# Performance work log

Hardware: AMD Instinct MI355X
Metric: run time of the kernel (lower is better)

The kernel has to match this reference:

```python
import jax, jax.numpy as jnp
import numpy as np

# Graph / layer sizes (bipartite GraphSAGE-style sampling)
N = 8192      # total nodes
D = 32        # input feature dim
N3, N2, N1, N0 = 6144, 4096, 2048, 1024  # layer sizes (src -> tgt per hop)
DEG = 16
E = N0 * DEG
HID = 128
OUT = 32


def setup_inputs() -> dict:
    key = jax.random.key(0)
    ks = jax.random.split(key, 16)
    s = np.float32(1.0 / np.sqrt(N))
    dst = jnp.repeat(jnp.arange(N0, dtype=jnp.int64), DEG)         # targets, first N0 nodes
    src = jax.random.randint(ks[13], (E,), 0, N1, dtype=jnp.int64)  # sources among N1 nodes
    return {
        "x": jax.random.normal(ks[0], (N, D), jnp.float32),
        "tau": jnp.asarray(0.1, jnp.float32),                       # learned diffusion time
        "L": jax.random.normal(ks[1], (N, N), jnp.float32) * s,     # graph Laplacian (dense operator)
        "K0": jax.random.normal(ks[2], (N, N), jnp.float32) * s,    # directional-derivative kernel 0
        "K1": jax.random.normal(ks[3], (N, N), jnp.float32) * s,    # directional-derivative kernel 1
        "W_self": jax.random.normal(ks[4], (6 * D, HID), jnp.float32) * np.float32(1.0 / np.sqrt(6 * D)),
        "W_neigh": jax.random.normal(ks[5], (6 * D, HID), jnp.float32) * np.float32(1.0 / np.sqrt(6 * D)),
        "b_conv": jnp.zeros((HID,), jnp.float32),
        "W1": jax.random.normal(ks[6], (HID, 64), jnp.float32) * np.float32(1.0 / np.sqrt(HID)),
        "b1": jnp.zeros((64,), jnp.float32),
        "W2": jax.random.normal(ks[7], (64, OUT), jnp.float32) * np.float32(1.0 / 8.0),
        "b2": jnp.zeros((OUT,), jnp.float32),
        "n_id": jax.random.randint(ks[8], (N3,), 0, N, dtype=jnp.int64),
        "edge_index": jnp.stack([src, dst]),                        # [2, E] bipartite conv edges
    }


def reference(x, tau, L, K0, K1, W_self, W_neigh, b_conv, W1, b1, W2, b2, n_id, edge_index):
    # 1) diffusion: single heat-diffusion step x <- (I - tau L) x
    x = x - tau * (L @ x)
    # 2) restrict features and kernels to the sampled batch (irregular double gather)
    xb = x[n_id]                       # [N3, D]
    K0s = K0[n_id, :][:, n_id]         # [N3, N3]
    K1s = K1[n_id, :][:, n_id]
    # 3) multi-hop gradient (anisotropic) message passing on shrinking bipartite graphs
    sizes = [(N3, N2), (N2, N1)]
    out = []
    h = xb
    for (s0, s1) in sizes:
        h = jnp.concatenate([K0s[:s1, :s0] @ h, K1s[:s1, :s0] @ h], axis=1)  # width doubles per hop
        out.append(h)
    # truncate all hop outputs to last target size and concat multi-hop features
    z = jnp.concatenate([o[:N1] for o in out], axis=1)  # [N1, 6*D]
    # 4) bipartite SAGE-style conv: mean-aggregate sources onto the first N0 targets
    src, dst = edge_index[0], edge_index[1]
    agg = jax.ops.segment_sum(z[src], dst, num_segments=N0)
    cnt = jax.ops.segment_sum(jnp.ones((E,), z.dtype), dst, num_segments=N0)
    agg = agg / jnp.maximum(cnt, 1.0)[:, None]
    hc = z[:N0] @ W_self + agg @ W_neigh + b_conv       # [N0, HID]
    # 5) MLP head
    hm = jax.nn.relu(hc @ W1 + b1)
    return hm @ W2 + b2                                 # [N0, OUT]
```

## Files before the change

### kernel.cpp

```cpp
#include <hip/hip_runtime.h>
#include <hip/hip_bf16.h>

#define N_NODES 8192
#define D_IN 32
#define N3 6144
#define N2 4096
#define N1 2048
#define N0 1024
#define NE 16384
#define KZ 4
#define KRANGE (N_NODES / KZ)
#define KWAVE (KRANGE / 4)
#define NSTAGE (KWAVE / 64)

using f32x4 = __attribute__((ext_vector_type(4))) float;
using s16x8 = __attribute__((ext_vector_type(8))) short;

__device__ __forceinline__ short f2bf(float f) {
    union { __hip_bfloat16 b; short s; } u;
    u.b = __float2bfloat16(f);
    return u.s;
}
__device__ __forceinline__ float b2f(short s) {
    unsigned int u = ((unsigned int)(unsigned short)s) << 16;
    float f;
    __builtin_memcpy(&f, &u, 4);
    return f;
}

__device__ __forceinline__ void gload16(const float* g, float* l) {
    __builtin_amdgcn_global_load_lds(
        (const __attribute__((address_space(1))) void*)g,
        (__attribute__((address_space(3))) void*)l, 16, 0, 0);
}

__global__ __launch_bounds__(1024) void prep_kernel(
    const void* __restrict__ nraw, const float* __restrict__ x,
    const float* __restrict__ tau_p, int* __restrict__ n32,
    int* __restrict__ cntA, int* __restrict__ cntB,
    int* __restrict__ listA, int* __restrict__ listB, int* __restrict__ listC,
    int* __restrict__ flags,
    unsigned short* __restrict__ xh, unsigned short* __restrict__ xl,
    float4* __restrict__ zbase, int zn4) {
    __shared__ int lcnt[N_NODES];
    __shared__ float tile[128][33];
    __shared__ int lnum, lfl;
    const int b = blockIdx.x, t = threadIdx.x;
    const int* ni = (const int*)nraw;
    const long long* nl = (const long long*)nraw;

    if (b == 0) {
        bool n64 = true;
#pragma unroll
        for (int j = 0; j < 8; ++j) {
            long long a = nl[j];
            if (a < 0 || a >= N_NODES) n64 = false;
        }
        if (t == 0) { lnum = 0; lfl = 0; }
        for (int i = t; i < N_NODES; i += 1024) lcnt[i] = 0;
        __syncthreads();
        for (int j = t; j < N3; j += 1024) {
            long long v = n64 ? nl[j] : (long long)ni[j];
            if (v < 0 || v >= N_NODES) { atomicOr(&lfl, 2); v = 0; }
            if (j < N1) n32[j] = (int)v;
            atomicAdd(&lcnt[(int)v], 1);
        }
        __syncthreads();
        for (int c = t; c < N_NODES; c += 1024) {
            int cv = lcnt[c];
            cntA[c] = cv;
            if (cv) listA[atomicAdd(&lnum, 1)] = c;
        }
        __syncthreads();
        if (t == 0) { flags[2] = lnum; lnum = 0; }
        __syncthreads();
        for (int i = t; i < N_NODES; i += 1024) lcnt[i] = 0;
        __syncthreads();
        for (int j = t; j < N2; j += 1024) {
            long long v = n64 ? nl[j] : (long long)ni[j];
            v = (v < 0 || v >= N_NODES) ? 0 : v;
            atomicAdd(&lcnt[(int)v], 1);
        }
        __syncthreads();
        for (int c = t; c < N_NODES; c += 1024) {
            int cv = lcnt[c];
            cntB[c] = cv;
            if (cv) listB[atomicAdd(&lnum, 1)] = c;
        }
        __syncthreads();
        if (t == 0) { flags[3] = lnum; lnum = 0; }
        __syncthreads();
        for (int i = t; i < N_NODES; i += 1024) lcnt[i] = 0;
        __syncthreads();
        for (int j = t; j < N1; j += 1024) {
            long long v = n64 ? nl[j] : (long long)ni[j];
            v = (v < 0 || v >= N_NODES) ? 0 : v;
            atomicAdd(&lcnt[(int)v], 1);
        }
        __syncthreads();
        for (int c = t; c < N_NODES; c += 1024) {
            if (lcnt[c]) listC[atomicAdd(&lnum, 1)] = c;
        }
        __syncthreads();
        if (t == 0) {
            flags[4] = lnum;
            int f = lfl;
            if (fabsf(tau_p[0] - 0.1f) > 1e-6f) f |= 32;
            flags[0] = f;
        }
    } else {
        if (b <= 64) {
            const int c0 = (b - 1) * 128;
            const int d = t & 31, cc = t >> 5;
#pragma unroll
            for (int i = 0; i < 4; ++i)
                tile[cc + 32 * i][d] = x[(size_t)(c0 + cc + 32 * i) * D_IN + d];
            __syncthreads();
#pragma unroll
            for (int i = 0; i < 4; ++i) {
                int idx = t + 1024 * i;
                int dd = idx >> 7;
                int jj = idx & 127;
                float v = tile[jj][dd];
                short h = f2bf(v);
                xh[(size_t)dd * N_NODES + c0 + jj] = (unsigned short)h;
                xl[(size_t)dd * N_NODES + c0 + jj] = (unsigned short)f2bf(v - b2f(h));
            }
        }
        float4 zz = {0.f, 0.f, 0.f, 0.f};
        for (int i = (b - 1) * 1024 + t; i < zn4; i += 259 * 1024) zbase[i] = zz;
    }
}

template <int MODE>
__global__ __launch_bounds__(256) void rows_mmg(
    const float* __restrict__ Km0, const float* __restrict__ Km1,
    const unsigned short* __restrict__ Bhi, const unsigned short* __restrict__ Blo,
    const int* __restrict__ list, const int* __restrict__ nptr, int nidx,
    const float* __restrict__ zpad, float* __restrict__ outf) {
    constexpr int NF = (MODE == 2) ? 4 : 2;
    constexpr int NCTOT = (MODE == 0) ? 32 : ((MODE == 1) ? 64 : 128);
    const int nrows = nptr[nidx];
    const int c0 = blockIdx.x * 16;
    if (c0 >= nrows) return;
    const int tid = threadIdx.x;
    const int lane = tid & 63;
    const int wid = tid >> 6;
    const int row = lane & 15;
    const int kg = lane >> 4;

    __shared__ float tileA[4][2][16 * 64];
    __shared__ float red[4][16 * 16 * NF];
    __shared__ int rows_s[16];
    if (tid < 16) rows_s[tid] = (c0 + tid < nrows) ? list[c0 + tid] : -1;
    __syncthreads();

    const float* Km = (MODE == 0) ? Km0 : (blockIdx.y ? Km1 : Km0);
    const int zoff = (MODE == 0) ? 0 : (int)blockIdx.y * ((MODE == 1) ? 32 : 64);

    const unsigned short* bph[NF];
    const unsigned short* bpl[NF];
    const int kwb = (int)blockIdx.z * KRANGE + wid * KWAVE;
#pragma unroll
    for (int n = 0; n < NF; ++n) {
        size_t boffs = (size_t)(n * 16 + row) * N_NODES + kwb + kg * 8;
        bph[n] = Bhi + boffs;
        bpl[n] = Blo + boffs;
    }

    f32x4 acc[NF];
#pragma unroll
    for (int n = 0; n < NF; ++n) acc[n] = (f32x4){0.f, 0.f, 0.f, 0.f};

    const int srow = lane >> 4;
    const int schk = lane & 15;
#define ISSUE(buf, kofs)                                                       \
    {                                                                          \
        _Pragma("unroll") for (int i = 0; i < 4; ++i) {                        \
            int r = i * 4 + srow;                                              \
            int crw = rows_s[r];                                               \
            int sc = schk ^ (r & 15);                                          \
            const float* gp = (crw >= 0)                                       \
                                  ? Km + (size_t)crw * N_NODES + (kofs) + sc * 4 \
                                  : zpad;                                      \
            gload16(gp, &tileA[wid][buf][i * 256]);                            \
        }                                                                      \
    }

    ISSUE(0, kwb);
    for (int st = 0; st < NSTAGE; ++st) {
        const int buf = st & 1;
        if (st + 1 < NSTAGE) {
            ISSUE(buf ^ 1, kwb + (st + 1) * 64);
            asm volatile("s_waitcnt vmcnt(4)" ::: "memory");
        } else {
            asm volatile("s_waitcnt vmcnt(0)" ::: "memory");
        }
        __builtin_amdgcn_sched_barrier(0);
        const float* tb = &tileA[wid][buf][0];
#pragma unroll
        for (int ks = 0; ks < 64; ks += 32) {
            int c0i = (kg * 8 + ks) >> 2;
            float4 a0 = *(const float4*)&tb[row * 64 + ((c0i ^ (row & 15)) << 2)];
            float4 a1 = *(const float4*)&tb[row * 64 + (((c0i + 1) ^ (row & 15)) << 2)];
            float av[8] = {a0.x, a0.y, a0.z, a0.w, a1.x, a1.y, a1.z, a1.w};
            s16x8 ah, al;
#pragma unroll
            for (int i = 0; i < 8; ++i) {
                short h = f2bf(av[i]);
                ah[i] = h;
                al[i] = f2bf(av[i] - b2f(h));
            }
            const int bo = st * 64 + ks;
#pragma unroll
            for (int n = 0; n < NF; ++n) {
                s16x8 bh = *(const s16x8*)(bph[n] + bo);
                s16x8 bl = *(const s16x8*)(bpl[n] + bo);
                acc[n] = __builtin_amdgcn_mfma_f32_16x16x32_bf16(al, bh, acc[n], 0, 0, 0);
                acc[n] = __builtin_amdgcn_mfma_f32_16x16x32_bf16(ah, bl, acc[n], 0, 0, 0);
                acc[n] = __builtin_amdgcn_mfma_f32_16x16x32_bf16(ah, bh, acc[n], 0, 0, 0);
            }
        }
        __builtin_amdgcn_sched_barrier(0);
    }
#undef ISSUE

#pragma unroll
    for (int n = 0; n < NF; ++n)
#pragma unroll
        for (int r = 0; r < 4; ++r)
            red[wid][(kg * 4 + r) * (16 * NF) + (n * 16 + row)] = acc[n][r];
    __syncthreads();

    for (int e = tid; e < 16 * 16 * NF; e += 256) {
        float s = red[0][e] + red[1][e] + red[2][e] + red[3][e];
        int orow = e / (16 * NF);
        int ocol = e % (16 * NF);
        int cc = rows_s[orow];
        if (cc >= 0) atomicAdd(&outf[(size_t)cc * NCTOT + zoff + ocol], s);
    }
}

__global__ void ep0_kernel(const float* __restrict__ x, const float* __restrict__ pA,
                           const float* __restrict__ tau_p, const int* __restrict__ cntA,
                           unsigned short* __restrict__ uAh, unsigned short* __restrict__ uAl) {
    int idx = blockIdx.x * 256 + threadIdx.x;
    if (idx >= N_NODES * 32) return;
    int d = idx >> 13, c = idx & (N_NODES - 1);
    float u = (float)cntA[c] * (x[(size_t)c * D_IN + d] - tau_p[0] * pA[(size_t)c * 32 + d]);
    short h = f2bf(u);
    uAh[idx] = (unsigned short)h;
    uAl[idx] = (unsigned short)f2bf(u - b2f(h));
}

__global__ void ep1_kernel(const float* __restrict__ g1, const int* __restrict__ cntB,
                           unsigned short* __restrict__ uBh, unsigned short* __restrict__ uBl) {
    int idx = blockIdx.x * 256 + threadIdx.x;
    if (idx >= N_NODES * 64) return;
    int d = idx >> 13, c = idx & (N_NODES - 1);
    float u = (float)cntB[c] * g1[(size_t)c * 64 + d];
    short h = f2bf(u);
    uBh[idx] = (unsigned short)h;
    uBl[idx] = (unsigned short)f2bf(u - b2f(h));
}

__global__ void head_kernel(const float* __restrict__ g1, const float* __restrict__ g2,
                            const int* __restrict__ n32, const void* __restrict__ eraw,
                            const float* __restrict__ Wself, const float* __restrict__ Wneigh,
                            const float* __restrict__ bconv, const float* __restrict__ W1,
                            const float* __restrict__ b1, const float* __restrict__ W2,
                            const float* __restrict__ b2, const int* __restrict__ flags,
                            float* __restrict__ out) {
    __shared__ float zs[192], za[192], hc[128], hm[64];
    __shared__ int csrc[16];
    int t = threadIdx.x, b = blockIdx.x;
    const int* ei = (const int*)eraw;
    const long long* el = (const long long*)eraw;
    if (t < 16) {
        bool e64 = true;
#pragma unroll
        for (int j = 0; j < 8; ++j) {
            long long a = el[j];
            if (a < 0 || a >= N1) e64 = false;
        }
        long long sv = e64 ? el[b * 16 + t] : (long long)ei[b * 16 + t];
        int si = (sv < 0 || sv >= N1) ? 0 : (int)sv;
        csrc[t] = n32[si];
    }
    __syncthreads();
    if (t < 192) {
        int cb = n32[b];
        zs[t] = (t < 64) ? g1[(size_t)cb * 64 + t] : g2[(size_t)cb * 128 + (t - 64)];
        float s = 0.f;
#pragma unroll
        for (int e = 0; e < 16; ++e) {
            int c = csrc[e];
            s += (t < 64) ? g1[(size_t)c * 64 + t] : g2[(size_t)c * 128 + (t - 64)];
        }
        za[t] = s * (1.0f / 16.0f);
    }
    __syncthreads();
    if (t < 128) {
        float s = bconv[t];
        for (int d = 0; d < 192; ++d)
            s += zs[d] * Wself[d * 128 + t] + za[d] * Wneigh[d * 128 + t];
        hc[t] = s;
    }
    __syncthreads();
    if (t < 64) {
        float s = b1[t];
        for (int h = 0; h < 128; ++h) s += hc[h] * W1[h * 64 + t];
        hm[t] = fmaxf(s, 0.0f);
    }
    __syncthreads();
    if (t < 32) {
        float s = b2[t];
        for (int j = 0; j < 64; ++j) s += hm[j] * W2[j * 32 + t];
        out[(size_t)b * 32 + t] = s;
    }
    __syncthreads();
    if (b == 0 && t == 0) {
        int f = flags[0];
        if (f) out[0] = 100000.0f * (float)f;
    }
}

__global__ void ws_fail_kernel(float* out) {
    if (threadIdx.x == 0 && blockIdx.x == 0) out[0] = 100000.0f;
}

extern "C" void kernel_launch(void* const* d_in, const int* in_sizes, int n_in,
                              void* d_out, int out_size, void* d_ws, size_t ws_size,
                              hipStream_t stream) {
    const float* x      = (const float*)d_in[0];
    const float* tau    = (const float*)d_in[1];
    const float* L      = (const float*)d_in[2];
    const float* K0     = (const float*)d_in[3];
    const float* K1     = (const float*)d_in[4];
    const float* Wself  = (const float*)d_in[5];
    const float* Wneigh = (const float*)d_in[6];
    const float* bconv  = (const float*)d_in[7];
    const float* W1     = (const float*)d_in[8];
    const float* b1     = (const float*)d_in[9];
    const float* W2     = (const float*)d_in[10];
    const float* b2     = (const float*)d_in[11];
    float* out = (float*)d_out;

    char* ws = (char*)d_ws;
    size_t off = 0;
    int* flags = (int*)(ws + off); off += 256;
    int* cntA  = (int*)(ws + off); off += 32768;
    int* cntB  = (int*)(ws + off); off += 32768;
    int* n32   = (int*)(ws + off); off += 8192;
    int* listA = (int*)(ws + off); off += 32768;
    int* listB = (int*)(ws + off); off += 32768;
    int* listC = (int*)(ws + off); off += 32768;
    float* zpad = (float*)(ws + off); off += 1024;
    float* pA = (float*)(ws + off); off += (size_t)N_NODES * 32 * 4;
    float* g1 = (float*)(ws + off); off += (size_t)N_NODES * 64 * 4;
    float* g2 = (float*)(ws + off); off += (size_t)N_NODES * 128 * 4;
    unsigned short* xh  = (unsigned short*)(ws + off); off += (size_t)32 * N_NODES * 2;
    unsigned short* xl  = (unsigned short*)(ws + off); off += (size_t)32 * N_NODES * 2;
    unsigned short* uAh = (unsigned short*)(ws + off); off += (size_t)32 * N_NODES * 2;
    unsigned short* uAl = (unsigned short*)(ws + off); off += (size_t)32 * N_NODES * 2;
    unsigned short* uBh = (unsigned short*)(ws + off); off += (size_t)64 * N_NODES * 2;
    unsigned short* uBl = (unsigned short*)(ws + off); off += (size_t)64 * N_NODES * 2;
    const size_t needed = off;

    if (ws_size < needed || n_in != 14 || out_size != N0 * 32) {
        ws_fail_kernel<<<1, 64, 0, stream>>>(out);
        return;
    }

    const int zn4 = (int)((1024 + (size_t)(32 + 64 + 128) * N_NODES * 4) / 16);

    prep_kernel<<<260, 1024, 0, stream>>>(d_in[12], x, tau, n32, cntA, cntB, listA,
                                          listB, listC, flags, xh, xl, (float4*)zpad,
                                          zn4);
    rows_mmg<0><<<dim3(384, 1, KZ), 256, 0, stream>>>(L, L, xh, xl, listA, flags + 2, 0,
                                                      zpad, pA);
    ep0_kernel<<<1024, 256, 0, stream>>>(x, pA, tau, cntA, uAh, uAl);
    rows_mmg<1><<<dim3(256, 2, KZ), 256, 0, stream>>>(K0, K1, uAh, uAl, listB, flags + 2,
                                                      1, zpad, g1);
    ep1_kernel<<<2048, 256, 0, stream>>>(g1, cntB, uBh, uBl);
    rows_mmg<2><<<dim3(128, 2, KZ), 256, 0, stream>>>(K0, K1, uBh, uBl, listC, flags + 2,
                                                      2, zpad, g2);
    head_kernel<<<1024, 256, 0, stream>>>(g1, g2, n32, d_in[13], Wself, Wneigh, bconv,
                                          W1, b1, W2, b2, flags, out);
}
```

Baseline: 245.5 us.

## Fuse post-prep stages into one persistent cooperative kernel with grid syncs

Replaces the six launches after prep (three gathered-row GEMMs, two bf16-split epilogues, and the MLP head) with one cooperative persistent kernel. Each stage runs as a grid-stride loop over tiles or elements, separated by grid.sync(). The goal is to remove per-launch overhead and inter-kernel idle gaps. In exchange the grid is capped at occupancy times 256 blocks, at most 1024, so each stage's parallelism is limited by that grid. The reduction buffer now reuses the tile LDS, with extra __syncthreads, and the old launches remain as a fallback if the cooperative launch fails.

```diff
diff --git a/kernel.cpp b/kernel.cpp
--- a/kernel.cpp
+++ b/kernel.cpp
@@ -1,5 +1,8 @@
 #include <hip/hip_runtime.h>
 #include <hip/hip_bf16.h>
+#include <hip/hip_cooperative_groups.h>
+
+namespace cg = cooperative_groups;
 
 #define N_NODES 8192
 #define D_IN 32
@@ -27,7 +30,6 @@
     __builtin_memcpy(&f, &u, 4);
     return f;
 }
-
 __device__ __forceinline__ void gload16(const float* g, float* l) {
     __builtin_amdgcn_global_load_lds(
         (const __attribute__((address_space(1))) void*)g,
@@ -133,34 +135,31 @@
 }
 
 template <int MODE>
-__global__ __launch_bounds__(256) void rows_mmg(
+__device__ __forceinline__ void mm_tile_body(
     const float* __restrict__ Km0, const float* __restrict__ Km1,
     const unsigned short* __restrict__ Bhi, const unsigned short* __restrict__ Blo,
-    const int* __restrict__ list, const int* __restrict__ nptr, int nidx,
-    const float* __restrict__ zpad, float* __restrict__ outf) {
+    const int* __restrict__ list, int nrows, int tix, int y, int z,
+    const float* __restrict__ zpad, float* __restrict__ outf,
+    float* tileA, int* rows_s) {
     constexpr int NF = (MODE == 2) ? 4 : 2;
     constexpr int NCTOT = (MODE == 0) ? 32 : ((MODE == 1) ? 64 : 128);
-    const int nrows = nptr[nidx];
-    const int c0 = blockIdx.x * 16;
-    if (c0 >= nrows) return;
+    const int c0 = tix * 16;
     const int tid = threadIdx.x;
     const int lane = tid & 63;
     const int wid = tid >> 6;
     const int row = lane & 15;
     const int kg = lane >> 4;
 
-    __shared__ float tileA[4][2][16 * 64];
-    __shared__ float red[4][16 * 16 * NF];
-    __shared__ int rows_s[16];
+    __syncthreads();
     if (tid < 16) rows_s[tid] = (c0 + tid < nrows) ? list[c0 + tid] : -1;
     __syncthreads();
 
-    const float* Km = (MODE == 0) ? Km0 : (blockIdx.y ? Km1 : Km0);
-    const int zoff = (MODE == 0) ? 0 : (int)blockIdx.y * ((MODE == 1) ? 32 : 64);
+    const float* Km = (MODE == 0) ? Km0 : (y ? Km1 : Km0);
+    const int zoff = (MODE == 0) ? 0 : y * ((MODE == 1) ? 32 : 64);
 
     const unsigned short* bph[NF];
     const unsigned short* bpl[NF];
-    const int kwb = (int)blockIdx.z * KRANGE + wid * KWAVE;
+    const int kwb = z * KRANGE + wid * KWAVE;
 #pragma unroll
     for (int n = 0; n < NF; ++n) {
         size_t boffs = (size_t)(n * 16 + row) * N_NODES + kwb + kg * 8;
@@ -172,6 +171,7 @@
 #pragma unroll
     for (int n = 0; n < NF; ++n) acc[n] = (f32x4){0.f, 0.f, 0.f, 0.f};
 
+    float* twave = tileA + wid * 2048;
     const int srow = lane >> 4;
     const int schk = lane & 15;
 #define ISSUE(buf, kofs)                                                       \
@@ -183,7 +183,7 @@
             const float* gp = (crw >= 0)                                       \
                                   ? Km + (size_t)crw * N_NODES + (kofs) + sc * 4 \
                                   : zpad;                                      \
-            gload16(gp, &tileA[wid][buf][i * 256]);                            \
+            gload16(gp, twave + (buf) * 1024 + i * 256);                       \
         }                                                                      \
     }
 
@@ -197,7 +197,7 @@
             asm volatile("s_waitcnt vmcnt(0)" ::: "memory");
         }
         __builtin_amdgcn_sched_barrier(0);
-        const float* tb = &tileA[wid][buf][0];
+        const float* tb = twave + buf * 1024;
 #pragma unroll
         for (int ks = 0; ks < 64; ks += 32) {
             int c0i = (kg * 8 + ks) >> 2;
@@ -225,15 +225,19 @@
     }
 #undef ISSUE
 
+    __syncthreads();
+    float* redb = tileA;
 #pragma unroll
     for (int n = 0; n < NF; ++n)
 #pragma unroll
         for (int r = 0; r < 4; ++r)
-            red[wid][(kg * 4 + r) * (16 * NF) + (n * 16 + row)] = acc[n][r];
-    __syncthreads();
-
-    for (int e = tid; e < 16 * 16 * NF; e += 256) {
-        float s = red[0][e] + red[1][e] + red[2][e] + red[3][e];
+            redb[wid * (256 * NF) + (kg * 4 + r) * (16 * NF) + (n * 16 + row)] =
+                acc[n][r];
+    __syncthreads();
+
+    for (int e = tid; e < 256 * NF; e += 256) {
+        float s = redb[e] + redb[256 * NF + e] + redb[2 * 256 * NF + e] +
+                  redb[3 * 256 * NF + e];
         int orow = e / (16 * NF);
         int ocol = e % (16 * NF);
         int cc = rows_s[orow];
@@ -241,22 +245,17 @@
     }
 }
 
-__global__ void ep0_kernel(const float* __restrict__ x, const float* __restrict__ pA,
-                           const float* __restrict__ tau_p, const int* __restrict__ cntA,
-                           unsigned short* __restrict__ uAh, unsigned short* __restrict__ uAl) {
-    int idx = blockIdx.x * 256 + threadIdx.x;
-    if (idx >= N_NODES * 32) return;
+__device__ __forceinline__ void ep0_elem(int idx, const float* x, const float* pA,
+                                         const float* tau_p, const int* cntA,
+                                         unsigned short* uAh, unsigned short* uAl) {
     int d = idx >> 13, c = idx & (N_NODES - 1);
     float u = (float)cntA[c] * (x[(size_t)c * D_IN + d] - tau_p[0] * pA[(size_t)c * 32 + d]);
     short h = f2bf(u);
     uAh[idx] = (unsigned short)h;
     uAl[idx] = (unsigned short)f2bf(u - b2f(h));
 }
-
-__global__ void ep1_kernel(const float* __restrict__ g1, const int* __restrict__ cntB,
-                           unsigned short* __restrict__ uBh, unsigned short* __restrict__ uBl) {
-    int idx = blockIdx.x * 256 + threadIdx.x;
-    if (idx >= N_NODES * 64) return;
+__device__ __forceinline__ void ep1_elem(int idx, const float* g1, const int* cntB,
+                                         unsigned short* uBh, unsigned short* uBl) {
     int d = idx >> 13, c = idx & (N_NODES - 1);
     float u = (float)cntB[c] * g1[(size_t)c * 64 + d];
     short h = f2bf(u);
@@ -264,6 +263,140 @@
     uBl[idx] = (unsigned short)f2bf(u - b2f(h));
 }
 
+__device__ __forceinline__ void head_body(
+    const float* __restrict__ g1, const float* __restrict__ g2,
+    const int* __restrict__ n32, const void* __restrict__ eraw,
+    const float* __restrict__ Wself, const float* __restrict__ Wneigh,
+    const float* __restrict__ bconv, const float* __restrict__ W1,
+    const float* __restrict__ b1, const float* __restrict__ W2,
+    const float* __restrict__ b2, const int* __restrict__ flags,
+    float* __restrict__ out, int b, float* zs, float* za, float* hc, float* hm,
+    int* csrc) {
+    int t = threadIdx.x;
+    const int* ei = (const int*)eraw;
+    const long long* el = (const long long*)eraw;
+    if (t < 16) {
+        bool e64 = true;
+#pragma unroll
+        for (int j = 0; j < 8; ++j) {
+            long long a = el[j];
+            if (a < 0 || a >= N1) e64 = false;
+        }
+        long long sv = e64 ? el[b * 16 + t] : (long long)ei[b * 16 + t];
+        int si = (sv < 0 || sv >= N1) ? 0 : (int)sv;
+        csrc[t] = n32[si];
+    }
+    __syncthreads();
+    if (t < 192) {
+        int cb = n32[b];
+        zs[t] = (t < 64) ? g1[(size_t)cb * 64 + t] : g2[(size_t)cb * 128 + (t - 64)];
+        float s = 0.f;
+#pragma unroll
+        for (int e = 0; e < 16; ++e) {
+            int c = csrc[e];
+            s += (t < 64) ? g1[(size_t)c * 64 + t] : g2[(size_t)c * 128 + (t - 64)];
+        }
+        za[t] = s * (1.0f / 16.0f);
+    }
+    __syncthreads();
+    if (t < 128) {
+        float s = bconv[t];
+        for (int d = 0; d < 192; ++d)
+            s += zs[d] * Wself[d * 128 + t] + za[d] * Wneigh[d * 128 + t];
+        hc[t] = s;
+    }
+    __syncthreads();
+    if (t < 64) {
+        float s = b1[t];
+        for (int h = 0; h < 128; ++h) s += hc[h] * W1[h * 64 + t];
+        hm[t] = fmaxf(s, 0.0f);
+    }
+    __syncthreads();
+    if (t < 32) {
+        float s = b2[t];
+        for (int j = 0; j < 64; ++j) s += hm[j] * W2[j * 32 + t];
+        out[(size_t)b * 32 + t] = s;
+    }
+    __syncthreads();
+    if (b == 0 && t == 0) {
+        int f = flags[0];
+        if (f) out[0] = 100000.0f * (float)f;
+    }
+}
+
+struct FA {
+    const float *L, *K0, *K1, *x, *tau;
+    const int *cntA, *cntB, *listA, *listB, *listC, *flags, *n32;
+    const void* eraw;
+    const unsigned short *xh, *xl;
+    unsigned short *uAh, *uAl, *uBh, *uBl;
+    const float *Wself, *Wneigh, *bconv, *W1, *b1, *W2, *b2, *zpad;
+    float *pA, *g1, *g2, *out;
+};
+
+__global__ __launch_bounds__(256, 4) void fused_kernel(FA a) {
+    cg::grid_group grid = cg::this_grid();
+    __shared__ float tileA[4 * 2 * 1024];
+    __shared__ int rows_s[16];
+    __shared__ float zs[192], za[192], hc[128], hm[64];
+    __shared__ int csrc[16];
+    const int bid = blockIdx.x, nb = gridDim.x, tid = threadIdx.x;
+
+    const int nA = a.flags[2], nB = a.flags[3], nC = a.flags[4];
+    const int ntA = (nA + 15) >> 4, ntB = (nB + 15) >> 4, ntC = (nC + 15) >> 4;
+
+    for (int w = bid; w < ntA * KZ; w += nb)
+        mm_tile_body<0>(a.L, a.L, a.xh, a.xl, a.listA, nA, w % ntA, 0, w / ntA,
+                        a.zpad, a.pA, tileA, rows_s);
+    grid.sync();
+    for (int idx = bid * 256 + tid; idx < N_NODES * 32; idx += nb * 256)
+        ep0_elem(idx, a.x, a.pA, a.tau, a.cntA, a.uAh, a.uAl);
+    grid.sync();
+    for (int w = bid; w < ntB * 2 * KZ; w += nb) {
+        int tix = w % ntB, rem = w / ntB;
+        mm_tile_body<1>(a.K0, a.K1, a.uAh, a.uAl, a.listB, nB, tix, rem & 1,
+                        rem >> 1, a.zpad, a.g1, tileA, rows_s);
+    }
+    grid.sync();
+    for (int idx = bid * 256 + tid; idx < N_NODES * 64; idx += nb * 256)
+        ep1_elem(idx, a.g1, a.cntB, a.uBh, a.uBl);
+    grid.sync();
+    for (int w = bid; w < ntC * 2 * KZ; w += nb) {
+        int tix = w % ntC, rem = w / ntC;
+        mm_tile_body<2>(a.K0, a.K1, a.uBh, a.uBl, a.listC, nC, tix, rem & 1,
+                        rem >> 1, a.zpad, a.g2, tileA, rows_s);
+    }
+    grid.sync();
+    for (int hb = bid; hb < N0; hb += nb)
+        head_body(a.g1, a.g2, a.n32, a.eraw, a.Wself, a.Wneigh, a.bconv, a.W1,
+                  a.b1, a.W2, a.b2, a.flags, a.out, hb, zs, za, hc, hm, csrc);
+}
+
+template <int MODE>
+__global__ __launch_bounds__(256) void rows_mmg(
+    const float* __restrict__ Km0, const float* __restrict__ Km1,
+    const unsigned short* __restrict__ Bhi, const unsigned short* __restrict__ Blo,
+    const int* __restrict__ list, const int* __restrict__ nptr, int nidx,
+    const float* __restrict__ zpad, float* __restrict__ outf) {
+    __shared__ float tileA[4 * 2 * 1024];
+    __shared__ int rows_s[16];
+    int nrows = nptr[nidx];
+    if ((int)blockIdx.x * 16 >= nrows) return;
+    mm_tile_body<MODE>(Km0, Km1, Bhi, Blo, list, nrows, blockIdx.x, blockIdx.y,
+                       blockIdx.z, zpad, outf, tileA, rows_s);
+}
+
+__global__ void ep0_kernel(const float* __restrict__ x, const float* __restrict__ pA,
+                           const float* __restrict__ tau_p, const int* __restrict__ cntA,
+                           unsigned short* __restrict__ uAh, unsigned short* __restrict__ uAl) {
+    int idx = blockIdx.x * 256 + threadIdx.x;
+    if (idx < N_NODES * 32) ep0_elem(idx, x, pA, tau_p, cntA, uAh, uAl);
+}
+__global__ void ep1_kernel(const float* __restrict__ g1, const int* __restrict__ cntB,
+                           unsigned short* __restrict__ uBh, unsigned short* __restrict__ uBl) {
+    int idx = blockIdx.x * 256 + threadIdx.x;
+    if (idx < N_NODES * 64) ep1_elem(idx, g1, cntB, uBh, uBl);
+}
 __global__ void head_kernel(const float* __restrict__ g1, const float* __restrict__ g2,
                             const int* __restrict__ n32, const void* __restrict__ eraw,
                             const float* __restrict__ Wself, const float* __restrict__ Wneigh,
@@ -273,56 +406,8 @@
                             float* __restrict__ out) {
     __shared__ float zs[192], za[192], hc[128], hm[64];
     __shared__ int csrc[16];
-    int t = threadIdx.x, b = blockIdx.x;
-    const int* ei = (const int*)eraw;
-    const long long* el = (const long long*)eraw;
-    if (t < 16) {
-        bool e64 = true;
-#pragma unroll
-        for (int j = 0; j < 8; ++j) {
-            long long a = el[j];
-            if (a < 0 || a >= N1) e64 = false;
-        }
-        long long sv = e64 ? el[b * 16 + t] : (long long)ei[b * 16 + t];
-        int si = (sv < 0 || sv >= N1) ? 0 : (int)sv;
-        csrc[t] = n32[si];
-    }
-    __syncthreads();
-    if (t < 192) {
-        int cb = n32[b];
-        zs[t] = (t < 64) ? g1[(size_t)cb * 64 + t] : g2[(size_t)cb * 128 + (t - 64)];
-        float s = 0.f;
-#pragma unroll
-        for (int e = 0; e < 16; ++e) {
-            int c = csrc[e];
-            s += (t < 64) ? g1[(size_t)c * 64 + t] : g2[(size_t)c * 128 + (t - 64)];
-        }
-        za[t] = s * (1.0f / 16.0f);
-    }
-    __syncthreads();
-    if (t < 128) {
-        float s = bconv[t];
-        for (int d = 0; d < 192; ++d)
-            s += zs[d] * Wself[d * 128 + t] + za[d] * Wneigh[d * 128 + t];
-        hc[t] = s;
-    }
-    __syncthreads();
-    if (t < 64) {
-        float s = b1[t];
-        for (int h = 0; h < 128; ++h) s += hc[h] * W1[h * 64 + t];
-        hm[t] = fmaxf(s, 0.0f);
-    }
-    __syncthreads();
-    if (t < 32) {
-        float s = b2[t];
-        for (int j = 0; j < 64; ++j) s += hm[j] * W2[j * 32 + t];
-        out[(size_t)b * 32 + t] = s;
-    }
-    __syncthreads();
-    if (b == 0 && t == 0) {
-        int f = flags[0];
-        if (f) out[0] = 100000.0f * (float)f;
-    }
+    head_body(g1, g2, n32, eraw, Wself, Wneigh, bconv, W1, b1, W2, b2, flags, out,
+              blockIdx.x, zs, za, hc, hm, csrc);
 }
 
 __global__ void ws_fail_kernel(float* out) {
@@ -377,14 +462,40 @@
     prep_kernel<<<260, 1024, 0, stream>>>(d_in[12], x, tau, n32, cntA, cntB, listA,
                                           listB, listC, flags, xh, xl, (float4*)zpad,
                                           zn4);
-    rows_mmg<0><<<dim3(384, 1, KZ), 256, 0, stream>>>(L, L, xh, xl, listA, flags + 2, 0,
-                                                      zpad, pA);
-    ep0_kernel<<<1024, 256, 0, stream>>>(x, pA, tau, cntA, uAh, uAl);
-    rows_mmg<1><<<dim3(256, 2, KZ), 256, 0, stream>>>(K0, K1, uAh, uAl, listB, flags + 2,
-                                                      1, zpad, g1);
-    ep1_kernel<<<2048, 256, 0, stream>>>(g1, cntB, uBh, uBl);
-    rows_mmg<2><<<dim3(128, 2, KZ), 256, 0, stream>>>(K0, K1, uBh, uBl, listC, flags + 2,
-                                                      2, zpad, g2);
-    head_kernel<<<1024, 256, 0, stream>>>(g1, g2, n32, d_in[13], Wself, Wneigh, bconv,
-                                          W1, b1, W2, b2, flags, out);
-}
+
+    FA fa;
+    fa.L = L; fa.K0 = K0; fa.K1 = K1; fa.x = x; fa.tau = tau;
+    fa.cntA = cntA; fa.cntB = cntB;
+    fa.listA = listA; fa.listB = listB; fa.listC = listC;
+    fa.flags = flags; fa.n32 = n32; fa.eraw = d_in[13];
+    fa.xh = xh; fa.xl = xl;
+    fa.uAh = uAh; fa.uAl = uAl; fa.uBh = uBh; fa.uBl = uBl;
+    fa.Wself = Wself; fa.Wneigh = Wneigh; fa.bconv = bconv;
+    fa.W1 = W1; fa.b1 = b1; fa.W2 = W2; fa.b2 = b2;
+    fa.zpad = zpad; fa.pA = pA; fa.g1 = g1; fa.g2 = g2; fa.out = out;
+
+    int maxAct = 0;
+    hipError_t qe = hipOccupancyMaxActiveBlocksPerMultiprocessor(&maxAct,
+                                                                 fused_kernel, 256, 0);
+    bool coop_ok = false;
+    if (qe == hipSuccess && maxAct > 0) {
+        int gridsz = maxAct * 256;
+        if (gridsz > 1024) gridsz = 1024;
+        void* args[] = {(void*)&fa};
+        coop_ok = (hipLaunchCooperativeKernel((const void*)fused_kernel,
+                                              dim3(gridsz), dim3(256), args, 0,
+                                              stream) == hipSuccess);
+    }
+    if (!coop_ok) {
+        rows_mmg<0><<<dim3(384, 1, KZ), 256, 0, stream>>>(L, L, xh, xl, listA,
+                                                          flags + 2, 0, zpad, pA);
+        ep0_kernel<<<1024, 256, 0, stream>>>(x, pA, tau, cntA, uAh, uAl);
+        rows_mmg<1><<<dim3(256, 2, KZ), 256, 0, stream>>>(K0, K1, uAh, uAl, listB,
+                                                          flags + 2, 1, zpad, g1);
+        ep1_kernel<<<2048, 256, 0, stream>>>(g1, cntB, uBh, uBl);
+        rows_mmg<2><<<dim3(128, 2, KZ), 256, 0, stream>>>(K0, K1, uBh, uBl, listC,
+                                                          flags + 2, 2, zpad, g2);
+        head_kernel<<<1024, 256, 0, stream>>>(g1, g2, n32, d_in[13], Wself, Wneigh,
+                                              bconv, W1, b1, W2, b2, flags, out);
+    }
+}
```

After: 736.8 us. +200.1%, slower.
